# Kernel tuning notes

Measured on AMD Instinct MI355X. Metric: run time of the kernel, lower is better.

## Reference

```python
import jax, jax.numpy as jnp
import numpy as np

HIDDEN = 2048
H = 16            # num heads
Q_RANK = 1536
KV_RANK = 512
D_NOPE = 128
D_ROPE = 64
D_QK = D_NOPE + D_ROPE   # 192
D_V = 128
ROPE_BASE = 10000.0
EPS = 1e-6


def _rms_norm(x, w):
    xf = x.astype(jnp.float32)
    var = jnp.mean(xf * xf, axis=-1, keepdims=True)
    return w * (xf * jax.lax.rsqrt(var + EPS)).astype(x.dtype)


def _rotate_half(x):
    x1, x2 = x[..., : x.shape[-1] // 2], x[..., x.shape[-1] // 2:]
    return jnp.concatenate((-x2, x1), axis=-1)


def _rope_cos_sin(position_ids, dtype):
    inv_freq = 1.0 / (ROPE_BASE ** (jnp.arange(0, D_ROPE, 2, dtype=jnp.float32) / D_ROPE))
    freqs = position_ids.astype(jnp.float32)[..., None] * inv_freq  # [b,s,32]
    emb = jnp.concatenate((freqs, freqs), axis=-1)                  # [b,s,64]
    return jnp.cos(emb).astype(dtype), jnp.sin(emb).astype(dtype)


def setup_inputs() -> dict:
    key = jax.random.key(0)
    ks = jax.random.split(key, 8)
    b, s = 1, 2048
    scale = 0.02
    return {
        "hidden_states": jax.random.normal(ks[0], (b, s, HIDDEN), jnp.float32),
        "position_ids": jnp.broadcast_to(jnp.arange(s, dtype=jnp.int64)[None, :], (b, s)),
        "q_a_w": jax.random.normal(ks[1], (Q_RANK, HIDDEN), jnp.float32) * scale,
        "q_a_ln_w": jnp.ones((Q_RANK,), jnp.float32),
        "q_b_w": jax.random.normal(ks[2], (H * D_QK, Q_RANK), jnp.float32) * scale,
        "kv_a_w": jax.random.normal(ks[3], (KV_RANK + D_ROPE, HIDDEN), jnp.float32) * scale,
        "kv_a_ln_w": jnp.ones((KV_RANK,), jnp.float32),
        "kv_b_w": jax.random.normal(ks[4], (H * (D_NOPE + D_V), KV_RANK), jnp.float32) * scale,
        "o_w": jax.random.normal(ks[5], (HIDDEN, H * D_V), jnp.float32) * scale,
    }


def reference(hidden_states, position_ids, q_a_w, q_a_ln_w, q_b_w, kv_a_w, kv_a_ln_w, kv_b_w, o_w):
    b, s, _ = hidden_states.shape
    softmax_scale = D_QK ** (-0.5)

    # Q path: low-rank down-proj -> RMSNorm -> up-proj
    q_a = hidden_states @ q_a_w.T                              # [b,s,q_rank]
    q = (_rms_norm(q_a, q_a_ln_w) @ q_b_w.T).reshape(b, s, H, D_QK)
    q_nope, q_pe = q[..., :D_NOPE], q[..., D_NOPE:]

    # KV path: joint down-proj -> split latent / rope part
    kv_a = hidden_states @ kv_a_w.T                            # [b,s,kv_rank+rope]
    compressed_kv = _rms_norm(kv_a[..., :KV_RANK], kv_a_ln_w)  # [b,s,kv_rank]
    k_pe = kv_a[..., KV_RANK:]                                 # [b,s,rope]
    kv_b = (compressed_kv @ kv_b_w.T).reshape(b, s, H, D_NOPE + D_V)
    k_nope, v = kv_b[..., :D_NOPE], kv_b[..., D_NOPE:]

    # decoupled RoPE on the rope slice
    cos, sin = _rope_cos_sin(position_ids, hidden_states.dtype)  # [b,s,64]
    cos, sin = cos[:, :, None, :], sin[:, :, None, :]            # [b,s,1,64]
    q_pe = q_pe * cos + _rotate_half(q_pe) * sin                 # [b,s,H,64]
    k_pe_h = jnp.broadcast_to(k_pe[:, :, None, :], (b, s, H, D_ROPE))
    k_pe_h = k_pe_h * cos + _rotate_half(k_pe_h) * sin

    q_full = jnp.concatenate([q_nope, q_pe], axis=-1)            # [b,s,H,192]
    k_full = jnp.concatenate([k_nope, k_pe_h], axis=-1)          # [b,s,H,192]

    # naive materialized attention (matches reference)
    scores = jnp.einsum("bqhd,bkhd->bhqk", q_full, k_full) * softmax_scale
    causal = jnp.triu(jnp.full((s, s), -jnp.inf, dtype=scores.dtype), k=1)
    scores = scores + causal
    probs = jax.nn.softmax(scores.astype(jnp.float32), axis=-1).astype(q_full.dtype)
    attn = jnp.einsum("bhqk,bkhd->bqhd", probs, v).reshape(b, s, H * D_V)
    return attn @ o_w.T
```

## Files before the change

kernel.cpp:

```cpp
#include <hip/hip_runtime.h>
#include <stdint.h>

#define S_LEN 2048
#define HIDDEN_ 2048
#define NH 16
#define QR 1536
#define KVR 512
#define DN 128
#define DR 64
#define DQK 192
#define DV 128
#define NQKV 2112

#define KT_STRIDE 6144
#define VT_STRIDE 4096

typedef __attribute__((ext_vector_type(8))) short bf16x8;
typedef __attribute__((ext_vector_type(4))) float f32x4;
typedef __attribute__((ext_vector_type(4))) unsigned short u16x4;
typedef unsigned short u16;
typedef unsigned int u32;

#define GLOAD_LDS16(g, l)                                                      \
    __builtin_amdgcn_global_load_lds(                                          \
        (const __attribute__((address_space(1))) void*)(g),                    \
        (__attribute__((address_space(3))) void*)(l), 16, 0, 0)

__device__ inline float bf2f(u16 x) {
    union { u32 u; float f; } v; v.u = ((u32)x) << 16; return v.f;
}
__device__ inline u16 f2bf(float f) {
    union { float f; u32 u; } v; v.f = f;
    u32 u = v.u;
    return (u16)((u + 0x7fffu + ((u >> 16) & 1u)) >> 16);
}

__global__ void cvt6(const float* __restrict__ s0, u16* __restrict__ d0, int n0,
                     const float* __restrict__ s1, u16* __restrict__ d1, int n1,
                     const float* __restrict__ s2, u16* __restrict__ d2, int n2,
                     const float* __restrict__ s3, u16* __restrict__ d3, int n3,
                     const float* __restrict__ s4, u16* __restrict__ d4, int n4,
                     const float* __restrict__ s5, u16* __restrict__ d5, int n5)
{
    const int b0 = n0 >> 10, b1 = n1 >> 10, b2 = n2 >> 10, b3 = n3 >> 10,
              b4 = n4 >> 10;
    int gid = blockIdx.x;
    const float* src; u16* dst; int base;
    if (gid < b0)                     { src = s0; dst = d0; base = gid; }
    else if ((gid -= b0) < b1)        { src = s1; dst = d1; base = gid; }
    else if ((gid -= b1) < b2)        { src = s2; dst = d2; base = gid; }
    else if ((gid -= b2) < b3)        { src = s3; dst = d3; base = gid; }
    else if ((gid -= b3) < b4)        { src = s4; dst = d4; base = gid; }
    else                              { src = s5; dst = d5; base = gid - b4; }
    int i = base * 1024 + threadIdx.x * 4;
    float4 v = *(const float4*)(src + i);
    u16x4 o;
    o[0] = f2bf(v.x); o[1] = f2bf(v.y); o[2] = f2bf(v.z); o[3] = f2bf(v.w);
    *(u16x4*)(dst + i) = o;
}

__device__ __forceinline__
void gemm_body(const u16* __restrict__ A, const u16* __restrict__ B,
               void* __restrict__ Cv, int M, int N, int Kloop, int ld,
               int out_f32, int bx, int by)
{
    __shared__ u16 sA[128 * 32];
    __shared__ u16 sB[128 * 32];
    const int tid  = threadIdx.x;
    const int wave = tid >> 6;
    const int lane = tid & 63;
    const int l16  = lane & 15;
    const int quad = lane >> 4;
    const int m_blk = by * 128;
    const int n_blk = bx * 128;
    const int wm = (wave >> 1) * 64;
    const int wn = (wave & 1) * 64;

    const f32x4 zero4 = {0.f, 0.f, 0.f, 0.f};
    f32x4 acc[4][4];
#pragma unroll
    for (int i = 0; i < 4; i++)
#pragma unroll
        for (int j = 0; j < 4; j++) acc[i][j] = zero4;

    const int srow = lane >> 2;
    const int scol = (lane & 3) * 8;

    for (int k0 = 0; k0 < Kloop; k0 += 32) {
        __syncthreads();
#pragma unroll
        for (int p = 0; p < 2; p++) {
            const int rbase = wave * 32 + p * 16;
            const int row = rbase + srow;
            const u16* ga = A + (size_t)(m_blk + row) * ld + k0 + scol;
            GLOAD_LDS16(ga, &sA[rbase * 32]);
            int brow = n_blk + row; if (brow >= N) brow = N - 1;
            const u16* gb = B + (size_t)brow * ld + k0 + scol;
            GLOAD_LDS16(gb, &sB[rbase * 32]);
        }
        __syncthreads();

        bf16x8 af[4], bfr[4];
#pragma unroll
        for (int i = 0; i < 4; i++)
            af[i] = *(const bf16x8*)(sA + (wm + i * 16 + l16) * 32 + quad * 8);
#pragma unroll
        for (int j = 0; j < 4; j++)
            bfr[j] = *(const bf16x8*)(sB + (wn + j * 16 + l16) * 32 + quad * 8);
#pragma unroll
        for (int i = 0; i < 4; i++)
#pragma unroll
            for (int j = 0; j < 4; j++)
                acc[i][j] = __builtin_amdgcn_mfma_f32_16x16x32_bf16(
                    af[i], bfr[j], acc[i][j], 0, 0, 0);
    }

#pragma unroll
    for (int i = 0; i < 4; i++)
#pragma unroll
        for (int j = 0; j < 4; j++)
#pragma unroll
            for (int r = 0; r < 4; r++) {
                int mrow = m_blk + wm + i * 16 + quad * 4 + r;
                int ncol = n_blk + wn + j * 16 + l16;
                if (ncol < N) {
                    if (out_f32)
                        ((float*)Cv)[(size_t)mrow * N + ncol] = acc[i][j][r];
                    else
                        ((u16*)Cv)[(size_t)mrow * N + ncol] = f2bf(acc[i][j][r]);
                }
            }
}

__global__ __launch_bounds__(256, 3)
void gemm_splitk(const u16* __restrict__ A, const u16* __restrict__ B,
                 float* __restrict__ C0, float* __restrict__ C1,
                 int M, int N, int Kh, int ld)
{
    float* C = blockIdx.z ? C1 : C0;
    gemm_body(A + (size_t)blockIdx.z * Kh, B + (size_t)blockIdx.z * Kh,
              C, M, N, Kh, ld, 1, blockIdx.x, blockIdx.y);
}

__global__ __launch_bounds__(256, 3)
void gemm_dual(const u16* A0, const u16* B0, u16* C0, int M0, int N0, int K0,
               const u16* A1, const u16* B1, u16* C1, int M1, int N1, int K1)
{
    if (blockIdx.z == 0) {
        if ((int)blockIdx.x >= (N0 + 127) / 128) return;
        gemm_body(A0, B0, C0, M0, N0, K0, K0, 0, blockIdx.x, blockIdx.y);
    } else {
        gemm_body(A1, B1, C1, M1, N1, K1, K1, 0, blockIdx.x, blockIdx.y);
    }
}

__global__ void rmsnorm2_k(const float* __restrict__ P0, const float* __restrict__ P1,
                           const float* __restrict__ W0, u16* __restrict__ Y0,
                           const float* __restrict__ W1, u16* __restrict__ Y1,
                           u16* __restrict__ kpe)
{
    const int row = blockIdx.x;
    const float* p0 = P0 + (size_t)row * NQKV;
    const float* p1 = P1 + (size_t)row * NQKV;
    __shared__ float xbuf[QR];
    __shared__ float red[4];
    int off, len; const float* W; u16* Y;
    if (blockIdx.y == 0) { off = 0;  len = QR;  W = W0; Y = Y0 + (size_t)row * QR;  }
    else                 { off = QR; len = KVR; W = W1; Y = Y1 + (size_t)row * KVR; }
    float ss = 0.f;
    for (int i = threadIdx.x; i < len; i += 256) {
        float v = p0[off + i] + p1[off + i];
        xbuf[i] = v;
        ss += v * v;
    }
#pragma unroll
    for (int o = 32; o; o >>= 1) ss += __shfl_down(ss, o, 64);
    if ((threadIdx.x & 63) == 0) red[threadIdx.x >> 6] = ss;
    __syncthreads();
    float tot = red[0] + red[1] + red[2] + red[3];
    float inv = 1.0f / sqrtf(tot / (float)len + 1e-6f);
    for (int i = threadIdx.x; i < len; i += 256)
        Y[i] = f2bf(W[i] * xbuf[i] * inv);
    if (blockIdx.y == 1 && threadIdx.x < DR) {
        int i = threadIdx.x;
        kpe[(size_t)row * DR + i] = f2bf(p0[QR + KVR + i] + p1[QR + KVR + i]);
    }
}

__global__ void repack_fused(const u16* __restrict__ q,
                             const u16* __restrict__ kvb,
                             const u16* __restrict__ kpe_b,
                             u16* __restrict__ Q, u16* __restrict__ Kf,
                             u16* __restrict__ Vt)
{
    __shared__ __align__(16) char smem[64 * 72 * 2];
    const int bid = blockIdx.x;
    const int t = threadIdx.x;

    if (bid < S_LEN) {
        float* cs = (float*)smem;
        float* sn = cs + 64;
        u16* kpe_r = (u16*)(sn + 64);
        const float QSC = 0.07216878364870323f * 1.4426950408889634f;
        const int s = bid;
        const float pos = (float)s;
        if (t < 64) {
            int jf = t & 31;
            float freq = powf(10000.f, -(float)(2 * jf) / 64.f);
            float ang = pos * freq;
            cs[t] = cosf(ang);
            sn[t] = sinf(ang);
        }
        __syncthreads();
        if (t < 64) {
            int j = t;
            float x = bf2f(kpe_b[(size_t)s * DR + j]);
            float other = (j < 32) ? -bf2f(kpe_b[(size_t)s * DR + j + 32])
                                   :  bf2f(kpe_b[(size_t)s * DR + j - 32]);
            kpe_r[j] = f2bf(x * cs[j] + other * sn[j]);
        }
        __syncthreads();

        for (int idx = t; idx < NH * 24; idx += 256) {
            const int h  = idx / 24;
            const int cg = idx % 24;
            const int d0v = cg * 8;
            const size_t qbase = (size_t)s * (NH * DQK) + h * DQK;
            bf16x8 qv, kv;
            if (d0v < DN) {
                bf16x8 qr = *(const bf16x8*)(q + qbase + d0v);
#pragma unroll
                for (int e = 0; e < 8; e++)
                    qv[e] = (short)f2bf(bf2f((u16)qr[e]) * QSC);
                kv = *(const bf16x8*)(kvb + (size_t)s * (NH * 256) + h * 256 + d0v);
            } else {
                const int j0 = d0v - DN;
#pragma unroll
                for (int e = 0; e < 8; e++) {
                    int j = j0 + e;
                    float x = bf2f(q[qbase + DN + j]);
                    float other = (j < 32) ? -bf2f(q[qbase + DN + j + 32])
                                           :  bf2f(q[qbase + DN + j - 32]);
                    qv[e] = (short)f2bf((x * cs[j] + other * sn[j]) * QSC);
                    kv[e] = (short)kpe_r[j];
                }
            }
            *(bf16x8*)&Q[((size_t)h * S_LEN + s) * DQK + d0v] = qv;
            const size_t koff = (size_t)(h * 64 + (s >> 5)) * KT_STRIDE
                              + (size_t)(cg * 32 + (s & 31)) * 8;
            *(bf16x8*)&Kf[koff] = kv;
        }
    } else {
        u16 (*tile)[72] = (u16(*)[72])smem;
        const int r   = bid - S_LEN;
        const int h   = r >> 6;
        const int rem = r & 63;
        const int s0  = (rem >> 1) * 64;
        const int d0  = (rem & 1) * 64;
#pragma unroll
        for (int p = 0; p < 2; p++) {
            int c = p * 256 + t;
            int rr = c >> 3, col = (c & 7) * 8;
            *(bf16x8*)&tile[rr][col] =
                *(const bf16x8*)&kvb[(size_t)(s0 + rr) * (NH * 256) + h * 256 + 128 + d0 + col];
        }
        __syncthreads();
#pragma unroll
        for (int p = 0; p < 2; p++) {
            int c = p * 256 + t;
            int dr = c >> 3, sc = (c & 7) * 8;
            bf16x8 v;
#pragma unroll
            for (int j = 0; j < 8; j++) v[j] = (short)tile[sc + j][dr];
            const int s_abs   = s0 + sc;
            const int kt      = s_abs >> 5;
            const int schunk  = (s_abs & 31) >> 3;
            const size_t voff = (size_t)(h * 64 + kt) * VT_STRIDE
                              + (size_t)(schunk * 128 + (d0 + dr)) * 8;
            *(bf16x8*)&Vt[voff] = v;
        }
    }
}

__global__ __launch_bounds__(256, 3)
void mla_attn(const u16* __restrict__ Q, const u16* __restrict__ Kf,
              const u16* __restrict__ Vt, u16* __restrict__ attn,
              float* __restrict__ part)
{
    const int lin = blockIdx.x + 48 * blockIdx.y;
    const int h   = ((lin & 7) << 1) | ((lin >> 3) & 1);
    const int bx  = lin >> 4;

    int s, tb, te, cIdx; bool direct;
    if (bx < 16)      { s = 16 + bx; tb = 0;  te = 32;        cIdx = 0; direct = false; }
    else if (bx < 32) { s = bx;      tb = 32; te = 2 * s + 2; cIdx = 1; direct = false; }
    else              { s = 47 - bx; tb = 0;  te = 2 * s + 2; cIdx = 0; direct = true;  }

    const int wave  = threadIdx.x >> 6;
    const int lane  = threadIdx.x & 63;
    const int l16   = lane & 15;
    const int quad  = lane >> 4;
    const int q0    = s * 64 + wave * 16;
    const int qrow  = q0 + l16;

    const u16* Qh  = Q  + (size_t)h * S_LEN * DQK;
    const u16* Kh  = Kf + (size_t)h * 64 * KT_STRIDE;
    const u16* Vth = Vt + (size_t)h * 64 * VT_STRIDE;

    __shared__ u16 sK[2][24 * 32 * 8];
    __shared__ u16 sV[2][4 * 128 * 8];

    bf16x8 qf[6];
#pragma unroll
    for (int st = 0; st < 6; st++)
        qf[st] = *(const bf16x8*)(Qh + (size_t)qrow * DQK + st * 32 + quad * 8);

    const f32x4 zero4 = {0.f, 0.f, 0.f, 0.f};
    f32x4 oacc[8];
#pragma unroll
    for (int t = 0; t < 8; t++) oacc[t] = zero4;
    float mrow = -INFINITY, lrow = 0.f;

    auto stage = [&](int buf, int kt) {
        const u16* kp = Kh + (size_t)kt * KT_STRIDE;
#pragma unroll
        for (int g = 0; g < 3; g++)
            GLOAD_LDS16(kp + (g * 256 + wave * 64 + lane) * 8,
                        &sK[buf][(g * 256 + wave * 64) * 8]);
        const u16* vp = Vth + (size_t)kt * VT_STRIDE;
#pragma unroll
        for (int g = 0; g < 2; g++)
            GLOAD_LDS16(vp + (g * 256 + wave * 64 + lane) * 8,
                        &sV[buf][(g * 256 + wave * 64) * 8]);
    };

    stage(0, tb);

    for (int kt = tb; kt < te; kt++) {
        const int c0  = kt * 32;
        const int cur = (kt - tb) & 1;
        __syncthreads();
        if (kt + 1 < te) stage(cur ^ 1, kt + 1);

        if (c0 <= q0 + 15) {
            f32x4 s0 = zero4, s1 = zero4;
            __builtin_amdgcn_s_setprio(1);
#pragma unroll
            for (int st = 0; st < 6; st++) {
                bf16x8 k0 = *(const bf16x8*)&sK[cur][((st * 4 + quad) * 32 + l16) * 8];
                bf16x8 k1 = *(const bf16x8*)&sK[cur][((st * 4 + quad) * 32 + 16 + l16) * 8];
                s0 = __builtin_amdgcn_mfma_f32_16x16x32_bf16(k0, qf[st], s0, 0, 0, 0);
                s1 = __builtin_amdgcn_mfma_f32_16x16x32_bf16(k1, qf[st], s1, 0, 0, 0);
            }
            __builtin_amdgcn_s_setprio(0);
            bf16x8 vfr[8];
#pragma unroll
            for (int t = 0; t < 8; t++)
                vfr[t] = *(const bf16x8*)&sV[cur][(quad * 128 + t * 16 + l16) * 8];

            const bool full = (c0 + 31 <= q0);
            float v0[4], v1[4];
#pragma unroll
            for (int r = 0; r < 4; r++) {
                v0[r] = s0[r];
                v1[r] = s1[r];
                if (!full) {
                    if (c0 + quad * 4 + r > qrow)      v0[r] = -INFINITY;
                    if (c0 + 16 + quad * 4 + r > qrow) v1[r] = -INFINITY;
                }
            }
            float lm = fmaxf(fmaxf(fmaxf(v0[0], v0[1]), fmaxf(v0[2], v0[3])),
                             fmaxf(fmaxf(v1[0], v1[1]), fmaxf(v1[2], v1[3])));
            lm = fmaxf(lm, __shfl_xor(lm, 16, 64));
            lm = fmaxf(lm, __shfl_xor(lm, 32, 64));

            float mref;
            if (__all(lm <= mrow + 11.5416f)) {
                mref = mrow;
            } else {
                mref = fmaxf(mrow, lm);
                const float alpha = __builtin_amdgcn_exp2f(mrow - mref);
#pragma unroll
                for (int t = 0; t < 8; t++) oacc[t] *= alpha;
                lrow *= alpha;
                mrow = mref;
            }

            float p0[4], p1[4], rs = 0.f;
#pragma unroll
            for (int r = 0; r < 4; r++) {
                p0[r] = __builtin_amdgcn_exp2f(v0[r] - mref);
                p1[r] = __builtin_amdgcn_exp2f(v1[r] - mref);
                rs += p0[r] + p1[r];
            }
            lrow += rs;

            u32 A0, A1, B0, B1;
            asm("v_cvt_pk_bf16_f32 %0, %1, %2" : "=v"(A0) : "v"(p0[0]), "v"(p0[1]));
            asm("v_cvt_pk_bf16_f32 %0, %1, %2" : "=v"(A1) : "v"(p0[2]), "v"(p0[3]));
            asm("v_cvt_pk_bf16_f32 %0, %1, %2" : "=v"(B0) : "v"(p1[0]), "v"(p1[1]));
            asm("v_cvt_pk_bf16_f32 %0, %1, %2" : "=v"(B1) : "v"(p1[2]), "v"(p1[3]));
            const int a0 = (((quad & 1) << 5) + l16) << 2;
            const int a1 = a0 + 64;
            u32 Y0 = (u32)__builtin_amdgcn_ds_bpermute(a0, (int)A0);
            u32 Y1 = (u32)__builtin_amdgcn_ds_bpermute(a0, (int)A1);
            u32 Y2 = (u32)__builtin_amdgcn_ds_bpermute(a1, (int)A0);
            u32 Y3 = (u32)__builtin_amdgcn_ds_bpermute(a1, (int)A1);
            u32 Z0 = (u32)__builtin_amdgcn_ds_bpermute(a0, (int)B0);
            u32 Z1 = (u32)__builtin_amdgcn_ds_bpermute(a0, (int)B1);
            u32 Z2 = (u32)__builtin_amdgcn_ds_bpermute(a1, (int)B0);
            u32 Z3 = (u32)__builtin_amdgcn_ds_bpermute(a1, (int)B1);
            const bool useA = quad < 2;
            union { u32 w[4]; bf16x8 v; } pf;
            pf.w[0] = useA ? Y0 : Z0;
            pf.w[1] = useA ? Y1 : Z1;
            pf.w[2] = useA ? Y2 : Z2;
            pf.w[3] = useA ? Y3 : Z3;
            bf16x8 pfrag = pf.v;

            __builtin_amdgcn_s_setprio(1);
#pragma unroll
            for (int t = 0; t < 8; t++)
                oacc[t] = __builtin_amdgcn_mfma_f32_16x16x32_bf16(vfr[t], pfrag,
                                                                  oacc[t], 0, 0, 0);
            __builtin_amdgcn_s_setprio(0);
        }
    }

    float lsum = lrow;
    lsum += __shfl_xor(lsum, 16, 64);
    lsum += __shfl_xor(lsum, 32, 64);

    if (direct) {
        const float linv = 1.0f / lsum;
#pragma unroll
        for (int t = 0; t < 8; t++) {
            u16x4 ov;
#pragma unroll
            for (int r = 0; r < 4; r++) ov[r] = f2bf(oacc[t][r] * linv);
            *(u16x4*)&attn[(size_t)qrow * (NH * DV) + h * DV + t * 16 + quad * 4] = ov;
        }
    } else {
        float* pout = part + ((size_t)(h * 16 + (s - 16)) * 2 + cIdx) * 8320;
        const int rowl = wave * 16 + l16;
#pragma unroll
        for (int t = 0; t < 8; t++) {
            float4 ov = {oacc[t][0], oacc[t][1], oacc[t][2], oacc[t][3]};
            *(float4*)&pout[(size_t)rowl * 128 + t * 16 + quad * 4] = ov;
        }
        if (quad == 0) {
            pout[8192 + rowl] = mrow;
            pout[8256 + rowl] = lsum;
        }
    }
}

__global__ void attn_combine(const float* __restrict__ part, u16* __restrict__ attn)
{
    const int h = blockIdx.y, sIdx = blockIdx.x;
    const int s = 16 + sIdx;
    const float* p0 = part + ((size_t)(h * 16 + sIdx) * 2 + 0) * 8320;
    const float* p1 = p0 + 8320;
    for (int e = threadIdx.x; e < 8192; e += 256) {
        int row = e >> 7, d = e & 127;
        float m0 = p0[8192 + row], m1 = p1[8192 + row];
        float l0 = p0[8256 + row], l1 = p1[8256 + row];
        float M  = fmaxf(m0, m1);
        float w0 = __builtin_amdgcn_exp2f(m0 - M);
        float w1 = __builtin_amdgcn_exp2f(m1 - M);
        float o  = (w0 * p0[e] + w1 * p1[e]) / (w0 * l0 + w1 * l1);
        attn[(size_t)(s * 64 + row) * (NH * DV) + h * DV + d] = f2bf(o);
    }
}

__global__ void addf2(const float* __restrict__ a, const float* __restrict__ b,
                      float* __restrict__ o, int n)
{
    int i = (blockIdx.x * 256 + threadIdx.x) * 4;
    if (i + 3 < n) {
        float4 va = *(const float4*)(a + i);
        float4 vb = *(const float4*)(b + i);
        float4 vo = {va.x + vb.x, va.y + vb.y, va.z + vb.z, va.w + vb.w};
        *(float4*)(o + i) = vo;
    }
}

extern "C" void kernel_launch(void* const* d_in, const int* in_sizes, int n_in,
                              void* d_out, int out_size, void* d_ws, size_t ws_size,
                              hipStream_t stream)
{
    const float* hid      = (const float*)d_in[0];
    const float* q_a_w    = (const float*)d_in[2];
    const float* q_a_ln_w = (const float*)d_in[3];
    const float* q_b_w    = (const float*)d_in[4];
    const float* kv_a_w   = (const float*)d_in[5];
    const float* kv_a_ln_w= (const float*)d_in[6];
    const float* kv_b_w   = (const float*)d_in[7];
    const float* o_w      = (const float*)d_in[8];

    char* base = (char*)d_ws;
    u16* qkvaw_b = (u16*)(base + 0);
    u16* qbw_b   = (u16*)(base + 8650752);
    u16* kvbw_b  = (u16*)(base + 18087936);
    u16* ow_b    = (u16*)(base + 22282240);
    u16* hid_b   = (u16*)(base + 30670848);
    float* P0    = (float*)(base + 39059456);
    float* P1    = (float*)(base + 56360960);
    u16* q_n     = (u16*)(base + 73662464);
    u16* ckv     = (u16*)(base + 79953920);
    u16* kpe_b   = (u16*)(base + 82051072);
    u16* qb      = (u16*)(base + 82313216);
    u16* kvb     = (u16*)(base + 94896128);
    u16* Qb      = (u16*)(base + 39059456);
    u16* Kb      = (u16*)(base + 51642368);
    u16* Vtb     = (u16*)(base + 64225280);
    u16* attnb   = (u16*)(base + 72613888);
    float* partb = (float*)(base + 94896128);
    float* PO0   = (float*)(base + 82313216);
    float* PO1   = (float*)(base + 99090432);

    cvt6<<<dim3(19072), 256, 0, stream>>>(
        hid,    hid_b,                          HIDDEN_ * S_LEN,
        q_a_w,  qkvaw_b,                        QR * HIDDEN_,
        kv_a_w, qkvaw_b + (size_t)QR * HIDDEN_, (KVR + DR) * HIDDEN_,
        q_b_w,  qbw_b,                          NH * DQK * QR,
        kv_b_w, kvbw_b,                         NH * 256 * KVR,
        o_w,    ow_b,                           HIDDEN_ * NH * DV);

    gemm_splitk<<<dim3((NQKV + 127) / 128, S_LEN / 128, 2), 256, 0, stream>>>(
        hid_b, qkvaw_b, P0, P1, S_LEN, NQKV, HIDDEN_ / 2, HIDDEN_);
    rmsnorm2_k<<<dim3(S_LEN, 2), 256, 0, stream>>>(
        P0, P1, q_a_ln_w, q_n, kv_a_ln_w, ckv, kpe_b);
    gemm_dual<<<dim3(32, S_LEN / 128, 2), 256, 0, stream>>>(
        q_n, qbw_b, qb,  S_LEN, NH * DQK, QR,
        ckv, kvbw_b, kvb, S_LEN, NH * 256, KVR);
    repack_fused<<<dim3(S_LEN + 1024), 256, 0, stream>>>(
        qb, kvb, kpe_b, Qb, Kb, Vtb);
    mla_attn<<<dim3(48, NH), 256, 0, stream>>>(Qb, Kb, Vtb, attnb, partb);
    attn_combine<<<dim3(16, NH), 256, 0, stream>>>(partb, attnb);
    gemm_splitk<<<dim3(HIDDEN_ / 128, S_LEN / 128, 2), 256, 0, stream>>>(
        attnb, ow_b, PO0, PO1, S_LEN, HIDDEN_, HIDDEN_ / 2, HIDDEN_);
    addf2<<<dim3((S_LEN * HIDDEN_) / 1024), 256, 0, stream>>>(
        PO0, PO1, (float*)d_out, S_LEN * HIDDEN_);
}
```

Before: 329.6 us.

## Pair two query tiles per 512-thread attention block to share K/V staging

The attention kernel now runs 512-thread blocks in which waves 0-3 handle query tile p and waves 4-7 handle tile p+16. The two tiles share each staged K/V tile in LDS, which cuts the global loads per K tile. The key-range split is rebalanced so the grid has 32 blocks per head instead of 48, while the partial-combine layout is kept. The cost is fewer, larger blocks with different occupancy, and the low waves sit idle for key tiles past their causal limit.

```diff
diff --git a/kernel.cpp b/kernel.cpp
--- a/kernel.cpp
+++ b/kernel.cpp
@@ -282,25 +282,25 @@
     }
 }
 
-__global__ __launch_bounds__(256, 3)
+__global__ __launch_bounds__(512, 2)
 void mla_attn(const u16* __restrict__ Q, const u16* __restrict__ Kf,
               const u16* __restrict__ Vt, u16* __restrict__ attn,
               float* __restrict__ part)
 {
-    const int lin = blockIdx.x + 48 * blockIdx.y;
+    const int lin = blockIdx.x + 32 * blockIdx.y;
     const int h   = ((lin & 7) << 1) | ((lin >> 3) & 1);
-    const int bx  = lin >> 4;
-
-    int s, tb, te, cIdx; bool direct;
-    if (bx < 16)      { s = 16 + bx; tb = 0;  te = 32;        cIdx = 0; direct = false; }
-    else if (bx < 32) { s = bx;      tb = 32; te = 2 * s + 2; cIdx = 1; direct = false; }
-    else              { s = 47 - bx; tb = 0;  te = 2 * s + 2; cIdx = 0; direct = true;  }
+    const int cix = lin >> 4;
+
+    int p, tb, te, cIdx;
+    if (cix < 16) { p = cix;      tb = 0;      te = p + 17;     cIdx = 0; }
+    else          { p = 31 - cix; tb = p + 17; te = 2 * p + 34; cIdx = 1; }
 
     const int wave  = threadIdx.x >> 6;
     const int lane  = threadIdx.x & 63;
     const int l16   = lane & 15;
     const int quad  = lane >> 4;
-    const int q0    = s * 64 + wave * 16;
+    const int sMine = (wave < 4) ? p : p + 16;
+    const int q0    = sMine * 64 + (wave & 3) * 16;
     const int qrow  = q0 + l16;
 
     const u16* Qh  = Q  + (size_t)h * S_LEN * DQK;
@@ -323,15 +323,12 @@
 
     auto stage = [&](int buf, int kt) {
         const u16* kp = Kh + (size_t)kt * KT_STRIDE;
-#pragma unroll
-        for (int g = 0; g < 3; g++)
-            GLOAD_LDS16(kp + (g * 256 + wave * 64 + lane) * 8,
-                        &sK[buf][(g * 256 + wave * 64) * 8]);
+        GLOAD_LDS16(kp + (wave * 64 + lane) * 8, &sK[buf][(wave * 64) * 8]);
+        if (wave < 4)
+            GLOAD_LDS16(kp + ((8 + wave) * 64 + lane) * 8,
+                        &sK[buf][((8 + wave) * 64) * 8]);
         const u16* vp = Vth + (size_t)kt * VT_STRIDE;
-#pragma unroll
-        for (int g = 0; g < 2; g++)
-            GLOAD_LDS16(vp + (g * 256 + wave * 64 + lane) * 8,
-                        &sV[buf][(g * 256 + wave * 64) * 8]);
+        GLOAD_LDS16(vp + (wave * 64 + lane) * 8, &sV[buf][(wave * 64) * 8]);
     };
 
     stage(0, tb);
@@ -431,18 +428,20 @@
     lsum += __shfl_xor(lsum, 16, 64);
     lsum += __shfl_xor(lsum, 32, 64);
 
-    if (direct) {
-        const float linv = 1.0f / lsum;
-#pragma unroll
-        for (int t = 0; t < 8; t++) {
-            u16x4 ov;
-#pragma unroll
-            for (int r = 0; r < 4; r++) ov[r] = f2bf(oacc[t][r] * linv);
-            *(u16x4*)&attn[(size_t)qrow * (NH * DV) + h * DV + t * 16 + quad * 4] = ov;
+    if (wave < 4) {
+        if (cIdx == 0) {
+            const float linv = 1.0f / lsum;
+#pragma unroll
+            for (int t = 0; t < 8; t++) {
+                u16x4 ov;
+#pragma unroll
+                for (int r = 0; r < 4; r++) ov[r] = f2bf(oacc[t][r] * linv);
+                *(u16x4*)&attn[(size_t)qrow * (NH * DV) + h * DV + t * 16 + quad * 4] = ov;
+            }
         }
     } else {
-        float* pout = part + ((size_t)(h * 16 + (s - 16)) * 2 + cIdx) * 8320;
-        const int rowl = wave * 16 + l16;
+        float* pout = part + ((size_t)(h * 16 + p) * 2 + cIdx) * 8320;
+        const int rowl = (wave & 3) * 16 + l16;
 #pragma unroll
         for (int t = 0; t < 8; t++) {
             float4 ov = {oacc[t][0], oacc[t][1], oacc[t][2], oacc[t][3]};
@@ -536,7 +535,7 @@
         ckv, kvbw_b, kvb, S_LEN, NH * 256, KVR);
     repack_fused<<<dim3(S_LEN + 1024), 256, 0, stream>>>(
         qb, kvb, kpe_b, Qb, Kb, Vtb);
-    mla_attn<<<dim3(48, NH), 256, 0, stream>>>(Qb, Kb, Vtb, attnb, partb);
+    mla_attn<<<dim3(32, NH), 512, 0, stream>>>(Qb, Kb, Vtb, attnb, partb);
     attn_combine<<<dim3(16, NH), 256, 0, stream>>>(partb, attnb);
     gemm_splitk<<<dim3(HIDDEN_ / 128, S_LEN / 128, 2), 256, 0, stream>>>(
         attnb, ow_b, PO0, PO1, S_LEN, HIDDEN_, HIDDEN_ / 2, HIDDEN_);
```

After: 344.3 us. 4.5% more time.
